# Optimization experiments

Measured on AMD Instinct MI355X. Metric: run time of the kernel, lower is better.

The kernel has to match this reference:

```python
import jax, jax.numpy as jnp
import numpy as np

B, S, H, D = 2, 2048, 16, 64
HID = H * D
THETA = 10000.0
SCALING_FACTOR = 1
NEG_INF = -1e9


def _rope_cos_sin(position_ids):
    # Llama RoPE: inv_freq over even dims, duplicated halves.
    inv_freq = 1.0 / (THETA ** (jnp.arange(0, D, 2, dtype=jnp.float32) / D))  # [D/2]
    freqs = position_ids.astype(jnp.float32)[..., None] * inv_freq            # [B,S,D/2]
    emb = jnp.concatenate([freqs, freqs], axis=-1)                            # [B,S,D]
    return jnp.cos(emb), jnp.sin(emb)


def _rotate_half(x):
    x1, x2 = jnp.split(x, 2, axis=-1)
    return jnp.concatenate([-x2, x1], axis=-1)


def setup_inputs() -> dict:
    key = jax.random.key(0)
    ks = jax.random.split(key, 6)
    return {
        "hidden_states": jax.random.normal(ks[0], (B, S, HID), dtype=jnp.float32),
        "info_embeddings": jax.random.normal(ks[1], (B, S, HID), dtype=jnp.float32) * 0.1,
        "Wq": jax.random.normal(ks[2], (HID, HID), dtype=jnp.float32) * 0.02,
        "Wk": jax.random.normal(ks[3], (HID, HID), dtype=jnp.float32) * 0.02,
        "Wv": jax.random.normal(ks[4], (HID, HID), dtype=jnp.float32) * 0.02,
        "Wo": jax.random.normal(ks[5], (HID, HID), dtype=jnp.float32) * 0.02,
        "position_ids": jnp.broadcast_to(jnp.arange(S, dtype=jnp.int64), (B, S)),
    }


def reference(hidden_states, info_embeddings, Wq, Wk, Wv, Wo, position_ids):
    b, s, _ = hidden_states.shape
    # projections -> [B,H,S,D]
    q = (hidden_states @ Wq).reshape(b, s, H, D).transpose(0, 2, 1, 3)
    k = (hidden_states @ Wk).reshape(b, s, H, D).transpose(0, 2, 1, 3)
    v = (hidden_states @ Wv).reshape(b, s, H, D).transpose(0, 2, 1, 3)
    # info embedding added to q and k (pre-RoPE)
    info = info_embeddings.reshape(b, s, H, D).transpose(0, 2, 1, 3)
    q = q + info
    k = k + info
    # rotary position embedding
    cos, sin = _rope_cos_sin(position_ids)
    cos = cos[:, None]  # [B,1,S,D]
    sin = sin[:, None]
    q = q * cos + _rotate_half(q) * sin
    k = k * cos + _rotate_half(k) * sin
    # eager attention with custom scaling
    scale = 1.0 / float(np.sqrt(SCALING_FACTOR * D))
    scores = jnp.einsum("bhqd,bhkd->bhqk", q, k) * scale  # [B,H,S,S]
    causal = jnp.tril(jnp.ones((s, s), dtype=bool))
    scores = scores + jnp.where(causal, 0.0, NEG_INF).astype(scores.dtype)
    probs = jax.nn.softmax(scores, axis=-1)  # dropout p=0 (eval)
    attn = jnp.einsum("bhqk,bhkd->bhqd", probs, v)
    attn = attn.transpose(0, 2, 1, 3).reshape(b, s, HID)
    return attn @ Wo
```

## Files before the change

### kernel.cpp

```cpp
#include <hip/hip_runtime.h>
#include <hip/hip_bf16.h>

#define HB 2
#define HS 2048
#define HH 16
#define HD 64
#define HIDN 1024
#define MROWS 4096

typedef __attribute__((ext_vector_type(8))) short s16x8;
typedef __attribute__((ext_vector_type(4))) float f32x4;
typedef unsigned short u16;

__device__ inline u16 f2bf(float f) {
  union { __hip_bfloat16 h; u16 u; } cvt;
  cvt.h = __float2bfloat16(f);
  return cvt.u;
}

__device__ __forceinline__ void gload16(const u16* g, u16* l) {
  __builtin_amdgcn_global_load_lds((const __attribute__((address_space(1))) void*)g,
                                   (__attribute__((address_space(3))) void*)l, 16, 0, 0);
}

__global__ __launch_bounds__(256) void k_cvt(const float* __restrict__ in, u16* __restrict__ out, int n) {
  int i = (blockIdx.x * 256 + threadIdx.x) * 4;
  if (i >= n) return;
  float4 a = *(const float4*)(in + i);
  ushort4 r;
  r.x = f2bf(a.x); r.y = f2bf(a.y); r.z = f2bf(a.z); r.w = f2bf(a.w);
  *(ushort4*)(out + i) = r;
}

__global__ __launch_bounds__(256) void k_transpose(const float* __restrict__ W0, const float* __restrict__ W1,
                                                   const float* __restrict__ W2, const float* __restrict__ W3,
                                                   u16* __restrict__ out) {
  const float* W = (blockIdx.z == 0) ? W0 : (blockIdx.z == 1) ? W1 : (blockIdx.z == 2) ? W2 : W3;
  u16* O = out + (size_t)blockIdx.z * HIDN * HIDN;
  __shared__ float tile[64][65];
  int k0 = blockIdx.y * 64, c0 = blockIdx.x * 64;
  #pragma unroll
  for (int i = 0; i < 16; ++i) {
    int id = threadIdx.x + i * 256;
    int r = id >> 6, c = id & 63;
    tile[r][c] = W[(size_t)(k0 + r) * HIDN + c0 + c];
  }
  __syncthreads();
  #pragma unroll
  for (int i = 0; i < 16; ++i) {
    int id = threadIdx.x + i * 256;
    int r = id >> 6, c = id & 63;
    O[(size_t)(c0 + r) * HIDN + k0 + c] = f2bf(tile[c][r]);
  }
}

#define BM 128
#define BN 128
#define BK 64
#define LDK 72

__global__ __launch_bounds__(256) void k_qkv(const u16* __restrict__ X, const u16* __restrict__ Wt,
                                             const float* __restrict__ info,
                                             u16* __restrict__ Qb, u16* __restrict__ Kb, u16* __restrict__ Vt) {
  __shared__ __align__(16) u16 smem[128 * 136];
  const int z = blockIdx.z;
  const u16* Bt = Wt + (size_t)z * HIDN * HIDN;
  const int tid = threadIdx.x;
  const int lane = tid & 63, wave = tid >> 6;
  const int wr = wave >> 1, wc = wave & 1;
  const int lg = lane >> 4, li = lane & 15;
  const int bm0 = blockIdx.y * BM, bn0 = blockIdx.x * BN;

  const int srow = lane >> 3;
  const int scol = (lane & 7) * 8;

  f32x4 acc[4][4];
  #pragma unroll
  for (int m = 0; m < 4; ++m)
    #pragma unroll
    for (int n = 0; n < 4; ++n) acc[m][n] = (f32x4){0.f, 0.f, 0.f, 0.f};

  for (int k0 = 0; k0 < HIDN; k0 += BK) {
    __syncthreads();
    #pragma unroll
    for (int c = 0; c < 4; ++c) {
      const int ci = wave * 4 + c;
      const int row = ci * 8 + srow;
      gload16(X  + (size_t)(bm0 + row) * HIDN + k0 + scol, &smem[ci * 512]);
      gload16(Bt + (size_t)(bn0 + row) * HIDN + k0 + scol, &smem[8192 + ci * 512]);
    }
    __syncthreads();
    #pragma unroll
    for (int kk = 0; kk < 2; ++kk) {
      s16x8 af[4], bfr[4];
      #pragma unroll
      for (int m = 0; m < 4; ++m) af[m]  = *(const s16x8*)(&smem[(wr * 64 + m * 16 + li) * 64 + kk * 32 + lg * 8]);
      #pragma unroll
      for (int n = 0; n < 4; ++n) bfr[n] = *(const s16x8*)(&smem[8192 + (wc * 64 + n * 16 + li) * 64 + kk * 32 + lg * 8]);
      __builtin_amdgcn_s_setprio(1);
      #pragma unroll
      for (int m = 0; m < 4; ++m)
        #pragma unroll
        for (int n = 0; n < 4; ++n)
          acc[m][n] = __builtin_amdgcn_mfma_f32_16x16x32_bf16(af[m], bfr[n], acc[m][n], 0, 0, 0);
      __builtin_amdgcn_s_setprio(0);
    }
  }

  if (z < 2) {
    u16* dst = (z == 0) ? Qb : Kb;
    #pragma unroll
    for (int m = 0; m < 4; ++m) {
      #pragma unroll
      for (int r = 0; r < 4; ++r) {
        int t = bm0 + wr * 64 + m * 16 + lg * 4 + r;
        int b = t >> 11, s = t & (HS - 1);
        #pragma unroll
        for (int n = 0; n < 2; ++n) {
          int c1 = bn0 + wc * 64 + n * 16 + li;
          float v1 = acc[m][n][r]     + info[(size_t)t * HIDN + c1];
          float v2 = acc[m][n + 2][r] + info[(size_t)t * HIDN + c1 + 32];
          int j = n * 16 + li;
          float invf = exp2f(-0.41524101186092030f * (float)j);
          float ang = (float)s * invf;
          float sn, cs;
          __sincosf(ang, &sn, &cs);
          float o1 = v1 * cs - v2 * sn;
          float o2 = v2 * cs + v1 * sn;
          if (z == 0) { o1 *= 0.18033688011f; o2 *= 0.18033688011f; }
          int h = c1 >> 6, d1 = c1 & 63;
          size_t base = ((size_t)(b * HH + h) * HS + s) * HD;
          dst[base + d1]      = f2bf(o1);
          dst[base + d1 + 32] = f2bf(o2);
        }
      }
    }
  } else {
    __syncthreads();
    #pragma unroll
    for (int m = 0; m < 4; ++m)
      #pragma unroll
      for (int n = 0; n < 4; ++n)
        #pragma unroll
        for (int r = 0; r < 4; ++r) {
          int cl = wc * 64 + n * 16 + li;
          int ml = wr * 64 + m * 16 + lg * 4 + r;
          smem[cl * 136 + ml] = f2bf(acc[m][n][r]);
        }
    __syncthreads();
    const int b = bm0 >> 11, s0 = bm0 & (HS - 1);
    #pragma unroll
    for (int p = 0; p < 8; ++p) {
      int id = tid + p * 256;
      int cl = id >> 4, m8 = (id & 15) * 8;
      int c = bn0 + cl;
      int h = c >> 6, d = c & 63;
      s16x8 v = *(const s16x8*)(&smem[cl * 136 + m8]);
      *(s16x8*)(&Vt[((size_t)(b * HH + h) * HD + d) * HS + s0 + m8]) = v;
    }
  }
}

__global__ __launch_bounds__(256) void k_attn(const u16* __restrict__ Qb, const u16* __restrict__ Kb,
                                              const u16* __restrict__ Vt, u16* __restrict__ attnOut) {
  __shared__ u16 Ks[64 * LDK];
  __shared__ u16 Vs[64 * LDK];
  __shared__ u16 Ps[4][16 * LDK];
  const int bh = blockIdx.y;
  const u16* Qh = Qb + (size_t)bh * HS * HD;
  const u16* Kh = Kb + (size_t)bh * HS * HD;
  const u16* Vh = Vt + (size_t)bh * HD * HS;
  const int tid = threadIdx.x;
  const int lane = tid & 63, wave = tid >> 6;
  const int lg = lane >> 4, li = lane & 15;
  const int b = bh >> 4, h = bh & 15;

  const int sr0 = tid >> 3,          sc0 = (tid & 7) * 8;
  const int sr1 = (tid + 256) >> 3,  sc1 = ((tid + 256) & 7) * 8;

  #pragma unroll
  for (int phase = 0; phase < 2; ++phase) {
    const int qt = (phase == 0) ? (31 - (int)blockIdx.x) : (int)blockIdx.x;
    const int q0 = qt * 64;
    const int ntiles = qt + 1;

    s16x8 qf[2];
    #pragma unroll
    for (int kk = 0; kk < 2; ++kk)
      qf[kk] = *(const s16x8*)(Qh + (size_t)(q0 + wave * 16 + li) * HD + kk * 32 + lg * 8);

    f32x4 o[4];
    #pragma unroll
    for (int n = 0; n < 4; ++n) o[n] = (f32x4){0.f, 0.f, 0.f, 0.f};
    float mrow = -3e38f, lrow = 0.f;

    uint4 rK0, rK1, rV0, rV1;
    rK0 = *(const uint4*)(Kh + (size_t)sr0 * HD + sc0);
    rK1 = *(const uint4*)(Kh + (size_t)sr1 * HD + sc1);
    rV0 = *(const uint4*)(Vh + (size_t)sr0 * HS + sc0);
    rV1 = *(const uint4*)(Vh + (size_t)sr1 * HS + sc1);

    for (int t = 0; t < ntiles; ++t) {
      __syncthreads();
      *(uint4*)(&Ks[sr0 * LDK + sc0]) = rK0;
      *(uint4*)(&Ks[sr1 * LDK + sc1]) = rK1;
      *(uint4*)(&Vs[sr0 * LDK + sc0]) = rV0;
      *(uint4*)(&Vs[sr1 * LDK + sc1]) = rV1;
      __syncthreads();
      if (t + 1 < ntiles) {
        const int kv1 = (t + 1) * 64;
        rK0 = *(const uint4*)(Kh + (size_t)(kv1 + sr0) * HD + sc0);
        rK1 = *(const uint4*)(Kh + (size_t)(kv1 + sr1) * HD + sc1);
        rV0 = *(const uint4*)(Vh + (size_t)sr0 * HS + kv1 + sc0);
        rV1 = *(const uint4*)(Vh + (size_t)sr1 * HS + kv1 + sc1);
      }

      f32x4 sc[4];
      #pragma unroll
      for (int n = 0; n < 4; ++n) sc[n] = (f32x4){0.f, 0.f, 0.f, 0.f};
      __builtin_amdgcn_s_setprio(1);
      #pragma unroll
      for (int kk = 0; kk < 2; ++kk) {
        #pragma unroll
        for (int n = 0; n < 4; ++n) {
          s16x8 kfr = *(const s16x8*)(&Ks[(n * 16 + li) * LDK + kk * 32 + lg * 8]);
          sc[n] = __builtin_amdgcn_mfma_f32_16x16x32_bf16(kfr, qf[kk], sc[n], 0, 0, 0);
        }
      }
      __builtin_amdgcn_s_setprio(0);

      if (t == ntiles - 1) {
        const int qrel = wave * 16 + li;
        #pragma unroll
        for (int n = 0; n < 4; ++n)
          #pragma unroll
          for (int r = 0; r < 4; ++r)
            if (n * 16 + lg * 4 + r > qrel) sc[n][r] = -1e9f;
      }

      float pmax = sc[0][0];
      #pragma unroll
      for (int n = 0; n < 4; ++n)
        #pragma unroll
        for (int r = 0; r < 4; ++r) pmax = fmaxf(pmax, sc[n][r]);
      pmax = fmaxf(pmax, __shfl_xor(pmax, 16));
      pmax = fmaxf(pmax, __shfl_xor(pmax, 32));

      if (!__all(pmax - mrow <= 11.5f)) {
        float mnew = fmaxf(mrow, pmax);
        float corr = exp2f(mrow - mnew);
        mrow = mnew;
        lrow *= corr;
        float corrq[4];
        #pragma unroll
        for (int r = 0; r < 4; ++r) corrq[r] = __shfl(corr, lg * 4 + r);
        #pragma unroll
        for (int n = 0; n < 4; ++n)
          #pragma unroll
          for (int r = 0; r < 4; ++r) o[n][r] *= corrq[r];
      }

      float psum = 0.f;
      #pragma unroll
      for (int n = 0; n < 4; ++n) {
        u16 pb[4];
        #pragma unroll
        for (int r = 0; r < 4; ++r) {
          float p = exp2f(sc[n][r] - mrow);
          psum += p;
          pb[r] = f2bf(p);
        }
        uint2 w;
        w.x = (unsigned)pb[0] | ((unsigned)pb[1] << 16);
        w.y = (unsigned)pb[2] | ((unsigned)pb[3] << 16);
        *(uint2*)(&Ps[wave][li * LDK + n * 16 + lg * 4]) = w;
      }
      psum += __shfl_xor(psum, 16);
      psum += __shfl_xor(psum, 32);
      lrow += psum;

      __builtin_amdgcn_s_setprio(1);
      #pragma unroll
      for (int kk = 0; kk < 2; ++kk) {
        s16x8 pf = *(const s16x8*)(&Ps[wave][li * LDK + kk * 32 + lg * 8]);
        #pragma unroll
        for (int n = 0; n < 4; ++n) {
          s16x8 vf = *(const s16x8*)(&Vs[(n * 16 + li) * LDK + kk * 32 + lg * 8]);
          o[n] = __builtin_amdgcn_mfma_f32_16x16x32_bf16(pf, vf, o[n], 0, 0, 0);
        }
      }
      __builtin_amdgcn_s_setprio(0);
    }

    float linv = 1.0f / lrow;
    float linvq[4];
    #pragma unroll
    for (int r = 0; r < 4; ++r) linvq[r] = __shfl(linv, lg * 4 + r);
    #pragma unroll
    for (int n = 0; n < 4; ++n)
      #pragma unroll
      for (int r = 0; r < 4; ++r) {
        int srow = q0 + wave * 16 + lg * 4 + r;
        attnOut[(size_t)(b * HS + srow) * HIDN + h * 64 + n * 16 + li] = f2bf(o[n][r] * linvq[r]);
      }
  }
}

__global__ __launch_bounds__(256) void k_out(const u16* __restrict__ A, const u16* __restrict__ Bt,
                                             float* __restrict__ out) {
  __shared__ __align__(16) u16 As[BM * 64];
  __shared__ __align__(16) u16 Bs[BN * 64];
  const int tid = threadIdx.x;
  const int lane = tid & 63, wave = tid >> 6;
  const int wr = wave >> 1, wc = wave & 1;
  const int lg = lane >> 4, li = lane & 15;
  const int bm0 = blockIdx.y * BM, bn0 = blockIdx.x * BN;

  const int srow = lane >> 3;
  const int scol = (lane & 7) * 8;

  f32x4 acc[4][4];
  #pragma unroll
  for (int m = 0; m < 4; ++m)
    #pragma unroll
    for (int n = 0; n < 4; ++n) acc[m][n] = (f32x4){0.f, 0.f, 0.f, 0.f};

  for (int k0 = 0; k0 < HIDN; k0 += BK) {
    __syncthreads();
    #pragma unroll
    for (int c = 0; c < 4; ++c) {
      const int ci = wave * 4 + c;
      const int row = ci * 8 + srow;
      gload16(A  + (size_t)(bm0 + row) * HIDN + k0 + scol, &As[ci * 512]);
      gload16(Bt + (size_t)(bn0 + row) * HIDN + k0 + scol, &Bs[ci * 512]);
    }
    __syncthreads();
    #pragma unroll
    for (int kk = 0; kk < 2; ++kk) {
      s16x8 af[4], bfr[4];
      #pragma unroll
      for (int m = 0; m < 4; ++m) af[m]  = *(const s16x8*)(&As[(wr * 64 + m * 16 + li) * 64 + kk * 32 + lg * 8]);
      #pragma unroll
      for (int n = 0; n < 4; ++n) bfr[n] = *(const s16x8*)(&Bs[(wc * 64 + n * 16 + li) * 64 + kk * 32 + lg * 8]);
      __builtin_amdgcn_s_setprio(1);
      #pragma unroll
      for (int m = 0; m < 4; ++m)
        #pragma unroll
        for (int n = 0; n < 4; ++n)
          acc[m][n] = __builtin_amdgcn_mfma_f32_16x16x32_bf16(af[m], bfr[n], acc[m][n], 0, 0, 0);
      __builtin_amdgcn_s_setprio(0);
    }
  }

  #pragma unroll
  for (int m = 0; m < 4; ++m)
    #pragma unroll
    for (int r = 0; r < 4; ++r) {
      int t = bm0 + wr * 64 + m * 16 + lg * 4 + r;
      #pragma unroll
      for (int n = 0; n < 4; ++n) {
        int c = bn0 + wc * 64 + n * 16 + li;
        out[(size_t)t * HIDN + c] = acc[m][n][r];
      }
    }
}

extern "C" void kernel_launch(void* const* d_in, const int* in_sizes, int n_in,
                              void* d_out, int out_size, void* d_ws, size_t ws_size,
                              hipStream_t stream) {
  const float* hs   = (const float*)d_in[0];
  const float* info = (const float*)d_in[1];
  const float* Wq   = (const float*)d_in[2];
  const float* Wk   = (const float*)d_in[3];
  const float* Wv   = (const float*)d_in[4];
  const float* Wo   = (const float*)d_in[5];
  float* out = (float*)d_out;

  char* ws = (char*)d_ws;
  u16* Xbf  = (u16*)(ws);
  u16* Wt   = (u16*)(ws + ((size_t)8  << 20));
  u16* Qb   = (u16*)(ws + ((size_t)16 << 20));
  u16* Kb   = (u16*)(ws + ((size_t)24 << 20));
  u16* Vt   = (u16*)(ws + ((size_t)32 << 20));
  u16* attn = Xbf;

  k_cvt<<<(MROWS * HIDN / 4 + 255) / 256, 256, 0, stream>>>(hs, Xbf, MROWS * HIDN);
  k_transpose<<<dim3(16, 16, 4), 256, 0, stream>>>(Wq, Wk, Wv, Wo, Wt);
  k_qkv<<<dim3(HIDN / BN, MROWS / BM, 3), 256, 0, stream>>>(Xbf, Wt, info, Qb, Kb, Vt);
  k_attn<<<dim3(16, HB * HH), 256, 0, stream>>>(Qb, Kb, Vt, attn);
  k_out<<<dim3(HIDN / BN, MROWS / BM), 256, 0, stream>>>(attn, Wt + (size_t)3 * HIDN * HIDN, out);
}
```

Baseline: 127.5 us.

## Restructure attention into 128-row query blocks with double-buffered K/V tiles

```diff
diff --git a/kernel.cpp b/kernel.cpp
--- a/kernel.cpp
+++ b/kernel.cpp
@@ -161,149 +161,151 @@
   }
 }
 
-__global__ __launch_bounds__(256) void k_attn(const u16* __restrict__ Qb, const u16* __restrict__ Kb,
-                                              const u16* __restrict__ Vt, u16* __restrict__ attnOut) {
-  __shared__ u16 Ks[64 * LDK];
-  __shared__ u16 Vs[64 * LDK];
-  __shared__ u16 Ps[4][16 * LDK];
-  const int bh = blockIdx.y;
+__global__ __launch_bounds__(512, 4) void k_attn(const u16* __restrict__ Qb, const u16* __restrict__ Kb,
+                                                 const u16* __restrict__ Vt, u16* __restrict__ attnOut) {
+  __shared__ u16 Ks[2][64 * LDK];
+  __shared__ u16 Vs[2][64 * LDK];
+  __shared__ u16 Ps[8][16 * LDK];
+  const int bidx = blockIdx.x;
+  const int bh = bidx & 31;
+  const int x  = bidx >> 5;
+  const int j  = (x < 8) ? x : 23 - x;
+  const int q0 = j * 128;
+  const int ntiles = 2 * j + 2;
+
   const u16* Qh = Qb + (size_t)bh * HS * HD;
   const u16* Kh = Kb + (size_t)bh * HS * HD;
   const u16* Vh = Vt + (size_t)bh * HD * HS;
   const int tid = threadIdx.x;
-  const int lane = tid & 63, wave = tid >> 6;
+  const int lane = tid & 63, w = tid >> 6;
   const int lg = lane >> 4, li = lane & 15;
   const int b = bh >> 4, h = bh & 15;
 
-  const int sr0 = tid >> 3,          sc0 = (tid & 7) * 8;
-  const int sr1 = (tid + 256) >> 3,  sc1 = ((tid + 256) & 7) * 8;
-
-  #pragma unroll
-  for (int phase = 0; phase < 2; ++phase) {
-    const int qt = (phase == 0) ? (31 - (int)blockIdx.x) : (int)blockIdx.x;
-    const int q0 = qt * 64;
-    const int ntiles = qt + 1;
-
-    s16x8 qf[2];
-    #pragma unroll
-    for (int kk = 0; kk < 2; ++kk)
-      qf[kk] = *(const s16x8*)(Qh + (size_t)(q0 + wave * 16 + li) * HD + kk * 32 + lg * 8);
-
-    f32x4 o[4];
-    #pragma unroll
-    for (int n = 0; n < 4; ++n) o[n] = (f32x4){0.f, 0.f, 0.f, 0.f};
-    float mrow = -3e38f, lrow = 0.f;
-
-    uint4 rK0, rK1, rV0, rV1;
-    rK0 = *(const uint4*)(Kh + (size_t)sr0 * HD + sc0);
-    rK1 = *(const uint4*)(Kh + (size_t)sr1 * HD + sc1);
-    rV0 = *(const uint4*)(Vh + (size_t)sr0 * HS + sc0);
-    rV1 = *(const uint4*)(Vh + (size_t)sr1 * HS + sc1);
-
-    for (int t = 0; t < ntiles; ++t) {
+  const int row8 = lane >> 3;
+  const int col8 = (lane & 7) * 8;
+
+  s16x8 qf[2];
+  #pragma unroll
+  for (int kk = 0; kk < 2; ++kk)
+    qf[kk] = *(const s16x8*)(Qh + (size_t)(q0 + w * 16 + li) * HD + kk * 32 + lg * 8);
+
+  f32x4 o[4];
+  #pragma unroll
+  for (int n = 0; n < 4; ++n) o[n] = (f32x4){0.f, 0.f, 0.f, 0.f};
+  float mrow = -3e38f, lrow = 0.f;
+
+  {
+    uint4 rK = *(const uint4*)(Kh + (size_t)(w * 8 + row8) * HD + col8);
+    uint4 rV = *(const uint4*)(Vh + (size_t)(w * 8 + row8) * HS + col8);
+    *(uint4*)(&Ks[0][(w * 8 + row8) * LDK + col8]) = rK;
+    *(uint4*)(&Vs[0][(w * 8 + row8) * LDK + col8]) = rV;
+  }
+  __syncthreads();
+
+  for (int t = 0; t < ntiles; ++t) {
+    const int cur = t & 1;
+    uint4 rK, rV;
+    const bool more = (t + 1 < ntiles);
+    if (more) {
+      const int kv1 = (t + 1) * 64;
+      rK = *(const uint4*)(Kh + (size_t)(kv1 + w * 8 + row8) * HD + col8);
+      rV = *(const uint4*)(Vh + (size_t)(w * 8 + row8) * HS + kv1 + col8);
+    }
+
+    f32x4 sc[4];
+    #pragma unroll
+    for (int n = 0; n < 4; ++n) sc[n] = (f32x4){0.f, 0.f, 0.f, 0.f};
+    __builtin_amdgcn_s_setprio(1);
+    #pragma unroll
+    for (int kk = 0; kk < 2; ++kk) {
+      #pragma unroll
+      for (int n = 0; n < 4; ++n) {
+        s16x8 kfr = *(const s16x8*)(&Ks[cur][(n * 16 + li) * LDK + kk * 32 + lg * 8]);
+        sc[n] = __builtin_amdgcn_mfma_f32_16x16x32_bf16(kfr, qf[kk], sc[n], 0, 0, 0);
+      }
+    }
+    __builtin_amdgcn_s_setprio(0);
+
+    if (t >= 2 * j) {
+      const int qglob = q0 + w * 16 + li;
+      #pragma unroll
+      for (int n = 0; n < 4; ++n)
+        #pragma unroll
+        for (int r = 0; r < 4; ++r)
+          if (t * 64 + n * 16 + lg * 4 + r > qglob) sc[n][r] = -1e9f;
+    }
+
+    float pmax = sc[0][0];
+    #pragma unroll
+    for (int n = 0; n < 4; ++n)
+      #pragma unroll
+      for (int r = 0; r < 4; ++r) pmax = fmaxf(pmax, sc[n][r]);
+    pmax = fmaxf(pmax, __shfl_xor(pmax, 16));
+    pmax = fmaxf(pmax, __shfl_xor(pmax, 32));
+
+    if (!__all(pmax - mrow <= 11.5f)) {
+      float mnew = fmaxf(mrow, pmax);
+      float corr = exp2f(mrow - mnew);
+      mrow = mnew;
+      lrow *= corr;
+      float corrq[4];
+      #pragma unroll
+      for (int r = 0; r < 4; ++r) corrq[r] = __shfl(corr, lg * 4 + r);
+      #pragma unroll
+      for (int n = 0; n < 4; ++n)
+        #pragma unroll
+        for (int r = 0; r < 4; ++r) o[n][r] *= corrq[r];
+    }
+
+    float psum = 0.f;
+    #pragma unroll
+    for (int n = 0; n < 4; ++n) {
+      u16 pb[4];
+      #pragma unroll
+      for (int r = 0; r < 4; ++r) {
+        float p = exp2f(sc[n][r] - mrow);
+        psum += p;
+        pb[r] = f2bf(p);
+      }
+      uint2 wv;
+      wv.x = (unsigned)pb[0] | ((unsigned)pb[1] << 16);
+      wv.y = (unsigned)pb[2] | ((unsigned)pb[3] << 16);
+      *(uint2*)(&Ps[w][li * LDK + n * 16 + lg * 4]) = wv;
+    }
+    psum += __shfl_xor(psum, 16);
+    psum += __shfl_xor(psum, 32);
+    lrow += psum;
+
+    __builtin_amdgcn_s_setprio(1);
+    #pragma unroll
+    for (int kk = 0; kk < 2; ++kk) {
+      s16x8 pf = *(const s16x8*)(&Ps[w][li * LDK + kk * 32 + lg * 8]);
+      #pragma unroll
+      for (int n = 0; n < 4; ++n) {
+        s16x8 vf = *(const s16x8*)(&Vs[cur][(n * 16 + li) * LDK + kk * 32 + lg * 8]);
+        o[n] = __builtin_amdgcn_mfma_f32_16x16x32_bf16(pf, vf, o[n], 0, 0, 0);
+      }
+    }
+    __builtin_amdgcn_s_setprio(0);
+
+    if (more) {
+      *(uint4*)(&Ks[cur ^ 1][(w * 8 + row8) * LDK + col8]) = rK;
+      *(uint4*)(&Vs[cur ^ 1][(w * 8 + row8) * LDK + col8]) = rV;
       __syncthreads();
-      *(uint4*)(&Ks[sr0 * LDK + sc0]) = rK0;
-      *(uint4*)(&Ks[sr1 * LDK + sc1]) = rK1;
-      *(uint4*)(&Vs[sr0 * LDK + sc0]) = rV0;
-      *(uint4*)(&Vs[sr1 * LDK + sc1]) = rV1;
-      __syncthreads();
-      if (t + 1 < ntiles) {
-        const int kv1 = (t + 1) * 64;
-        rK0 = *(const uint4*)(Kh + (size_t)(kv1 + sr0) * HD + sc0);
-        rK1 = *(const uint4*)(Kh + (size_t)(kv1 + sr1) * HD + sc1);
-        rV0 = *(const uint4*)(Vh + (size_t)sr0 * HS + kv1 + sc0);
-        rV1 = *(const uint4*)(Vh + (size_t)sr1 * HS + kv1 + sc1);
-      }
-
-      f32x4 sc[4];
-      #pragma unroll
-      for (int n = 0; n < 4; ++n) sc[n] = (f32x4){0.f, 0.f, 0.f, 0.f};
-      __builtin_amdgcn_s_setprio(1);
-      #pragma unroll
-      for (int kk = 0; kk < 2; ++kk) {
-        #pragma unroll
-        for (int n = 0; n < 4; ++n) {
-          s16x8 kfr = *(const s16x8*)(&Ks[(n * 16 + li) * LDK + kk * 32 + lg * 8]);
-          sc[n] = __builtin_amdgcn_mfma_f32_16x16x32_bf16(kfr, qf[kk], sc[n], 0, 0, 0);
-        }
-      }
-      __builtin_amdgcn_s_setprio(0);
-
-      if (t == ntiles - 1) {
-        const int qrel = wave * 16 + li;
-        #pragma unroll
-        for (int n = 0; n < 4; ++n)
-          #pragma unroll
-          for (int r = 0; r < 4; ++r)
-            if (n * 16 + lg * 4 + r > qrel) sc[n][r] = -1e9f;
-      }
-
-      float pmax = sc[0][0];
-      #pragma unroll
-      for (int n = 0; n < 4; ++n)
-        #pragma unroll
-        for (int r = 0; r < 4; ++r) pmax = fmaxf(pmax, sc[n][r]);
-      pmax = fmaxf(pmax, __shfl_xor(pmax, 16));
-      pmax = fmaxf(pmax, __shfl_xor(pmax, 32));
-
-      if (!__all(pmax - mrow <= 11.5f)) {
-        float mnew = fmaxf(mrow, pmax);
-        float corr = exp2f(mrow - mnew);
-        mrow = mnew;
-        lrow *= corr;
-        float corrq[4];
-        #pragma unroll
-        for (int r = 0; r < 4; ++r) corrq[r] = __shfl(corr, lg * 4 + r);
-        #pragma unroll
-        for (int n = 0; n < 4; ++n)
-          #pragma unroll
-          for (int r = 0; r < 4; ++r) o[n][r] *= corrq[r];
-      }
-
-      float psum = 0.f;
-      #pragma unroll
-      for (int n = 0; n < 4; ++n) {
-        u16 pb[4];
-        #pragma unroll
-        for (int r = 0; r < 4; ++r) {
-          float p = exp2f(sc[n][r] - mrow);
-          psum += p;
-          pb[r] = f2bf(p);
-        }
-        uint2 w;
-        w.x = (unsigned)pb[0] | ((unsigned)pb[1] << 16);
-        w.y = (unsigned)pb[2] | ((unsigned)pb[3] << 16);
-        *(uint2*)(&Ps[wave][li * LDK + n * 16 + lg * 4]) = w;
-      }
-      psum += __shfl_xor(psum, 16);
-      psum += __shfl_xor(psum, 32);
-      lrow += psum;
-
-      __builtin_amdgcn_s_setprio(1);
-      #pragma unroll
-      for (int kk = 0; kk < 2; ++kk) {
-        s16x8 pf = *(const s16x8*)(&Ps[wave][li * LDK + kk * 32 + lg * 8]);
-        #pragma unroll
-        for (int n = 0; n < 4; ++n) {
-          s16x8 vf = *(const s16x8*)(&Vs[(n * 16 + li) * LDK + kk * 32 + lg * 8]);
-          o[n] = __builtin_amdgcn_mfma_f32_16x16x32_bf16(pf, vf, o[n], 0, 0, 0);
-        }
-      }
-      __builtin_amdgcn_s_setprio(0);
-    }
-
-    float linv = 1.0f / lrow;
-    float linvq[4];
-    #pragma unroll
-    for (int r = 0; r < 4; ++r) linvq[r] = __shfl(linv, lg * 4 + r);
-    #pragma unroll
-    for (int n = 0; n < 4; ++n)
-      #pragma unroll
-      for (int r = 0; r < 4; ++r) {
-        int srow = q0 + wave * 16 + lg * 4 + r;
-        attnOut[(size_t)(b * HS + srow) * HIDN + h * 64 + n * 16 + li] = f2bf(o[n][r] * linvq[r]);
-      }
-  }
+    }
+  }
+
+  float linv = 1.0f / lrow;
+  float linvq[4];
+  #pragma unroll
+  for (int r = 0; r < 4; ++r) linvq[r] = __shfl(linv, lg * 4 + r);
+  #pragma unroll
+  for (int n = 0; n < 4; ++n)
+    #pragma unroll
+    for (int r = 0; r < 4; ++r) {
+      int srow = q0 + w * 16 + lg * 4 + r;
+      attnOut[(size_t)(b * HS + srow) * HIDN + h * 64 + n * 16 + li] = f2bf(o[n][r] * linvq[r]);
+    }
 }
 
 __global__ __launch_bounds__(256) void k_out(const u16* __restrict__ A, const u16* __restrict__ Bt,
@@ -387,6 +389,6 @@
   k_cvt<<<(MROWS * HIDN / 4 + 255) / 256, 256, 0, stream>>>(hs, Xbf, MROWS * HIDN);
   k_transpose<<<dim3(16, 16, 4), 256, 0, stream>>>(Wq, Wk, Wv, Wo, Wt);
   k_qkv<<<dim3(HIDN / BN, MROWS / BM, 3), 256, 0, stream>>>(Xbf, Wt, info, Qb, Kb, Vt);
-  k_attn<<<dim3(16, HB * HH), 256, 0, stream>>>(Qb, Kb, Vt, attn);
+  k_attn<<<dim3(512), 512, 0, stream>>>(Qb, Kb, Vt, attn);
   k_out<<<dim3(HIDN / BN, MROWS / BM), 256, 0, stream>>>(attn, Wt + (size_t)3 * HIDN * HIDN, out);
 }
```

After: 129.2 us. No clear change (+1.3%).
